# Kernel optimization log

Hardware: AMD Instinct MI355X
Metric: run time of the kernel (lower is better)

The kernel has to match this reference:

```python
import jax, jax.numpy as jnp
import numpy as np

FACTOR = 2
KERNEL_SIZE = 3
GAIN = 1


def _setup_kernel(k):
    k = np.asarray(k, dtype=np.float32)
    if k.ndim == 1:
        k = np.outer(k, k)
    k /= k.sum()
    return k


def _fir_kernel():
    # k = _setup_kernel([1,3,1]) * (gain * factor**2), shape [1,1,3,3]
    k = _setup_kernel([1, 3, 1]) * (GAIN * FACTOR ** 2)
    return jnp.asarray(k)[None, None]


def setup_inputs() -> dict:
    key = jax.random.key(0)
    k1, k2 = jax.random.split(key)
    x = jax.random.normal(k1, (16, 512, 64, 64), dtype=jnp.float32)
    w = jax.random.normal(k2, (256, 512, 3, 3), dtype=jnp.float32) * 0.05
    return {"x": x, "w": w}


def reference(x, w):
    fir = _fir_kernel()  # [1,1,3,3]
    # source uses self.k.shape[0] == 1 (unsqueezed leading dim) in the pad formula
    p = 1 - FACTOR + KERNEL_SIZE - 1          # = 1
    pad0 = (p + 1) // 2 + FACTOR - 1          # = 2
    pad1 = p // 2                              # = 0

    inC, outC, kh, kw = w.shape
    w = w.reshape(outC, inC, kh, kw)          # pure reshape (data reinterpretation), as in source

    # F.conv_transpose2d(x, w, stride=factor) == conv with lhs_dilation, flipped kernel,
    # in/out channel dims swapped, full padding (kh-1).
    w_conv = jnp.flip(w, axis=(2, 3)).transpose(1, 0, 2, 3)  # OIHW [inC, outC, kh, kw]
    x = jax.lax.conv_general_dilated(
        x, w_conv, window_strides=(1, 1),
        padding=((kh - 1, kh - 1), (kw - 1, kw - 1)),
        lhs_dilation=(FACTOR, FACTOR),
        dimension_numbers=('NCHW', 'OIHW', 'NCHW'))
    N, C, H, W = x.shape  # H = 2*H_in + 1 (odd)

    # zero-interleave block is a no-op: local factor == 1 when self.factor == 2
    x = jnp.pad(x, ((0, 0), (0, 0), (pad0, pad1), (pad0, pad1)))
    # depthwise FIR: fold channels into batch, conv with single-channel 3x3 filter
    x = x.reshape(N * C, 1, H + pad0 + pad1, W + pad0 + pad1)
    x = jax.lax.conv_general_dilated(
        x, fir, window_strides=(1, 1), padding='VALID',
        dimension_numbers=('NCHW', 'OIHW', 'NCHW'))
    x = x.reshape(N, C, H, W)

    if W % 2 != 0:  # static shape check, matches source's odd-size crop
        x = x[:, :, :W - 1, :W - 1]
    return x
```

## Files before the change

kernel.cpp:

```cpp
#include <hip/hip_runtime.h>
#include <hip/hip_bf16.h>


typedef __attribute__((ext_vector_type(8))) short short8;
typedef __attribute__((ext_vector_type(4))) float float4v;

#define XP_ELEMS ((size_t)16 * 65 * 65 * 512)
#define WP_ELEMS ((size_t)9 * 256 * 512)
#define YP_ELEMS ((size_t)4 * 16 * 256 * 4096)

__device__ __forceinline__ void gl_lds16(const __hip_bfloat16* g, __hip_bfloat16* l) {
    __builtin_amdgcn_global_load_lds(
        (const __attribute__((address_space(1))) void*)g,
        (__attribute__((address_space(3))) void*)l, 16, 0, 0);
}

__global__ __launch_bounds__(256) void zero_pad_kernel(__hip_bfloat16* __restrict__ xp) {
    int idx = blockIdx.x * 256 + (int)threadIdx.x;
    if (idx >= 16 * 65 * 512) return;
    int c = idx & 511;
    int t = (idx >> 9) % 65;
    int n = idx / (65 * 512);
    __hip_bfloat16 z = __float2bfloat16(0.f);
    xp[(((size_t)(n * 65) + 0) * 65 + t) * 512 + c] = z;
    xp[(((size_t)(n * 65) + t) * 65 + 0) * 512 + c] = z;
}

__global__ __launch_bounds__(256) void pack_w_kernel(
    const float* __restrict__ w, __hip_bfloat16* __restrict__ wp) {
    int idx = blockIdx.x * 256 + (int)threadIdx.x;
    int c  = idx & 511;
    int o  = (idx >> 9) & 255;
    int ab = idx >> 17;
    int a = ab / 3, b = ab % 3;
    wp[idx] = __float2bfloat16(w[((size_t)(c * 256 + o) * 3 + a) * 3 + b]);
}

__global__ __launch_bounds__(256) void pack_x_kernel(
    const float* __restrict__ x, __hip_bfloat16* __restrict__ xp) {
    int i = blockIdx.x;
    int n = blockIdx.y;
    int tid = (int)threadIdx.x;
    __shared__ float tile[64][65];
    for (int c0 = 0; c0 < 512; c0 += 64) {
        __syncthreads();
#pragma unroll
        for (int rr = 0; rr < 16; rr++) {
            int cl = (tid >> 6) * 16 + rr;
            int j = tid & 63;
            tile[cl][j] = x[(((size_t)(n * 512 + c0 + cl) * 64) + i) * 64 + j];
        }
        __syncthreads();
#pragma unroll
        for (int pass = 0; pass < 2; pass++) {
            int task = pass * 256 + tid;
            int j  = task >> 3;
            int cg = task & 7;
            union { short8 v; unsigned short h[8]; } u;
#pragma unroll
            for (int r = 0; r < 8; r++) {
                __hip_bfloat16 b = __float2bfloat16(tile[cg * 8 + r][j]);
                u.h[r] = *(unsigned short*)&b;
            }
            *(short8*)(xp + (((size_t)(n * 65) + i + 1) * 65 + (j + 1)) * 512 +
                       c0 + cg * 8) = u.v;
        }
    }
}

__global__ __launch_bounds__(256) void mfma_conv_kernel(
    const __hip_bfloat16* __restrict__ xp, const __hip_bfloat16* __restrict__ wp,
    __hip_bfloat16* __restrict__ yp) {
    const int p  = blockIdx.z, ph = p >> 1, pw = p & 1;
    const int o0 = blockIdx.x * 128;
    const int mt = blockIdx.y;
    const int n  = mt >> 5;
    const int i0 = (mt & 31) << 1;
    const int tid  = (int)threadIdx.x;
    const int wave = tid >> 6, lane = tid & 63;
    const int wm = wave & 1, wn = wave >> 1;
    const int lrow = lane & 15, quad = lane >> 4;
    const int m0j   = wave * 16 + (lane >> 2);
    const int klane = (lane & 3) * 8;

    __shared__ __align__(16) __hip_bfloat16 lA[128 * 32];
    __shared__ __align__(16) __hip_bfloat16 lB[128 * 32];

    float4v acc[4][4];
#pragma unroll
    for (int fm = 0; fm < 4; fm++)
#pragma unroll
        for (int fn = 0; fn < 4; fn++) acc[fm][fn] = (float4v)0.f;

    __hip_bfloat16* la0 = lA + wave * 512;
    __hip_bfloat16* la1 = lA + 2048 + wave * 512;
    __hip_bfloat16* lb0 = lB + wave * 512;
    __hip_bfloat16* lb1 = lB + 2048 + wave * 512;

    const int nrt = ph ? 1 : 2, nct = pw ? 1 : 2;
    for (int rt = 0; rt < nrt; rt++) {
        const int drp = ph ? 1 : rt;
        const int a   = ph ? 1 : (rt ? 0 : 2);
        for (int ct = 0; ct < nct; ct++) {
            const int dsp = pw ? 1 : ct;
            const int b   = pw ? 1 : (ct ? 0 : 2);
            const int ab  = a * 3 + b;
            const __hip_bfloat16* A0 =
                xp + (((size_t)(n * 65 + i0 + drp)) * 65 + m0j + dsp) * 512 + klane;
            const __hip_bfloat16* A1 = A0 + (size_t)65 * 512;
            const __hip_bfloat16* B0 =
                wp + ((size_t)(ab * 256 + o0 + m0j)) * 512 + klane;
            const __hip_bfloat16* B1 = B0 + (size_t)64 * 512;

            for (int c0 = 0; c0 < 512; c0 += 32) {
                __syncthreads();
                gl_lds16(A0 + c0, la0);
                gl_lds16(A1 + c0, la1);
                gl_lds16(B0 + c0, lb0);
                gl_lds16(B1 + c0, lb1);
                __syncthreads();
                short8 af[4], bv[4];
#pragma unroll
                for (int fm = 0; fm < 4; fm++)
                    af[fm] = *(const short8*)(lA + ((wm * 64 + fm * 16 + lrow) * 32 + quad * 8));
#pragma unroll
                for (int fn = 0; fn < 4; fn++)
                    bv[fn] = *(const short8*)(lB + ((wn * 64 + fn * 16 + lrow) * 32 + quad * 8));
#pragma unroll
                for (int fm = 0; fm < 4; fm++)
#pragma unroll
                    for (int fn = 0; fn < 4; fn++)
                        acc[fm][fn] = __builtin_amdgcn_mfma_f32_16x16x32_bf16(
                            af[fm], bv[fn], acc[fm][fn], 0, 0, 0);
            }
        }
    }

#pragma unroll
    for (int fm = 0; fm < 4; fm++) {
        int j0 = fm * 16 + quad * 4;
#pragma unroll
        for (int fn = 0; fn < 4; fn++) {
            int o = o0 + wn * 64 + fn * 16 + lrow;
            union { ushort4 v; __hip_bfloat16 h[4]; } u;
#pragma unroll
            for (int r = 0; r < 4; r++) u.h[r] = __float2bfloat16(acc[fm][fn][r]);
            *(ushort4*)(yp + (((size_t)(p * 4096 + n * 256 + o)) << 12) +
                        ((i0 + wm) << 6) + j0) = u.v;
        }
    }
}

__device__ __forceinline__ float bf_lo(unsigned u) { return __uint_as_float(u << 16); }
__device__ __forceinline__ float bf_hi(unsigned u) { return __uint_as_float(u & 0xffff0000u); }

__global__ __launch_bounds__(256) void fir_kernel(
    const __hip_bfloat16* __restrict__ yp, float* __restrict__ out) {
    const int no  = blockIdx.x;
    const int tid = (int)threadIdx.x;

    __shared__ __align__(16) unsigned short ylds[4 * 64 * 64];

    const unsigned short* ysrc = (const unsigned short*)yp;
#pragma unroll
    for (int k = 0; k < 8; k++) {
        int chunk = k * 256 + tid;
        int q   = chunk >> 9;
        int off = (chunk & 511) << 3;
        *(short8*)(ylds + q * 4096 + off) =
            *(const short8*)(ysrc + (((size_t)(q * 4096 + no)) << 12) + off);
    }
    __syncthreads();

    const unsigned* yw = (const unsigned*)ylds;

    const int qp = tid & 31;
    const int iw = tid >> 5;

    const float rw[2][2][2] = {{{0.4f, 0.4f}, {1.2f, 0.f}},
                               {{0.f, 1.2f}, {0.4f, 0.4f}}};

    for (int s = 0; s < 8; s++) {
        const int I = s * 8 + iw;

        float Y3[2][2][2][3];
#pragma unroll
        for (int q = 0; q < 4; q++) {
            int phh = q >> 1, pww = q & 1;
#pragma unroll
            for (int k = 0; k < 2; k++) {
                int ih = I - 1 + k;
                float c0 = 0.f, c1 = 0.f, c2 = 0.f;
                if (ih >= 0) {
                    const unsigned* row = yw + (q * 64 + ih) * 32;
                    unsigned wb = row[qp];
                    c1 = bf_lo(wb);
                    c2 = bf_hi(wb);
                    if (qp > 0) c0 = bf_hi(row[qp - 1]);
                }
                Y3[phh][pww][k][0] = c0;
                Y3[phh][pww][k][1] = c1;
                Y3[phh][pww][k][2] = c2;
            }
        }

        float res[2][4];
#pragma unroll
        for (int t = 0; t < 2; t++) {
            float cs[2][2][2];
#pragma unroll
            for (int phh = 0; phh < 2; phh++)
#pragma unroll
                for (int k = 0; k < 2; k++)
#pragma unroll
                    for (int ew = 0; ew < 2; ew++) {
                        float sv = 0.f;
#pragma unroll
                        for (int pww = 0; pww < 2; pww++)
#pragma unroll
                            for (int l = 0; l < 2; l++)
                                sv += rw[ew][pww][l] * Y3[phh][pww][k][t + l];
                        cs[phh][k][ew] = sv;
                    }
#pragma unroll
            for (int eh = 0; eh < 2; eh++)
#pragma unroll
                for (int ew = 0; ew < 2; ew++) {
                    float sv = 0.f;
#pragma unroll
                    for (int phh = 0; phh < 2; phh++)
#pragma unroll
                        for (int k = 0; k < 2; k++)
                            sv += rw[eh][phh][k] * cs[phh][k][ew];
                    res[eh][t * 2 + ew] = sv;
                }
        }

        size_t base = ((size_t)no << 14) + ((size_t)(2 * I) << 7) + 4 * qp;
        float4v v0 = {res[0][0], res[0][1], res[0][2], res[0][3]};
        float4v v1 = {res[1][0], res[1][1], res[1][2], res[1][3]};
        *(float4v*)(out + base)       = v0;
        *(float4v*)(out + base + 128) = v1;
    }
}

__global__ __launch_bounds__(256) void fused_direct_kernel(
    const float* __restrict__ x, const float* __restrict__ w,
    float* __restrict__ out) {
    int idx = blockIdx.x * 256 + (int)threadIdx.x;
    int w_ = idx & 127, h = (idx >> 7) & 127, no = idx >> 14;
    int o = no & 255, n = no >> 8;
    int I = h >> 1, J = w_ >> 1;
    const float fr0 = 0.4f, fr1 = 1.2f, fr2 = 0.4f;
    float gh[3][3]; int rh[3]; int nh;
    if ((h & 1) == 0) {
        nh = 3;
        rh[0] = I - 2; gh[0][0] = 0.f; gh[0][1] = 0.f; gh[0][2] = fr0;
        rh[1] = I - 1; gh[1][0] = fr0; gh[1][1] = fr1; gh[1][2] = fr2;
        rh[2] = I;     gh[2][0] = fr2; gh[2][1] = 0.f; gh[2][2] = 0.f;
    } else {
        nh = 2;
        rh[0] = I - 1; gh[0][0] = 0.f; gh[0][1] = fr0; gh[0][2] = fr1;
        rh[1] = I;     gh[1][0] = fr1; gh[1][1] = fr2; gh[1][2] = 0.f;
    }
    float gw[3][3]; int cw[3]; int nw;
    if ((w_ & 1) == 0) {
        nw = 3;
        cw[0] = J - 2; gw[0][0] = 0.f; gw[0][1] = 0.f; gw[0][2] = fr0;
        cw[1] = J - 1; gw[1][0] = fr0; gw[1][1] = fr1; gw[1][2] = fr2;
        cw[2] = J;     gw[2][0] = fr2; gw[2][1] = 0.f; gw[2][2] = 0.f;
    } else {
        nw = 2;
        cw[0] = J - 1; gw[0][0] = 0.f; gw[0][1] = fr0; gw[0][2] = fr1;
        cw[1] = J;     gw[1][0] = fr1; gw[1][1] = fr2; gw[1][2] = 0.f;
    }
    float acc = 0.f;
    for (int c = 0; c < 512; c++) {
        const float* xb = x + ((size_t)(n * 512 + c) << 12);
        const float* wb = w + (size_t)(c * 256 + o) * 9;
        float tmp[3][3];
#pragma unroll
        for (int dr = 0; dr < 3; dr++) tmp[dr][0] = tmp[dr][1] = tmp[dr][2] = 0.f;
        for (int dr = 0; dr < nh; dr++) {
            int r = rh[dr]; if (r < 0) continue;
            for (int ds = 0; ds < nw; ds++) {
                int s = cw[ds]; if (s < 0) continue;
                float xv = xb[(r << 6) + s];
                tmp[dr][0] += gw[ds][0] * xv;
                tmp[dr][1] += gw[ds][1] * xv;
                tmp[dr][2] += gw[ds][2] * xv;
            }
        }
#pragma unroll
        for (int a = 0; a < 3; a++) {
            float xg0 = 0.f, xg1 = 0.f, xg2 = 0.f;
            for (int dr = 0; dr < nh; dr++) {
                float g = gh[dr][a];
                xg0 += g * tmp[dr][0]; xg1 += g * tmp[dr][1]; xg2 += g * tmp[dr][2];
            }
            acc += xg0 * wb[a * 3] + xg1 * wb[a * 3 + 1] + xg2 * wb[a * 3 + 2];
        }
    }
    out[idx] = acc;
}

extern "C" void kernel_launch(void* const* d_in, const int* in_sizes, int n_in,
                              void* d_out, int out_size, void* d_ws, size_t ws_size,
                              hipStream_t stream)
{
    (void)in_sizes; (void)n_in; (void)out_size;
    const float* x = (const float*)d_in[0];
    const float* w = (const float*)d_in[1];
    float* out = (float*)d_out;

    const size_t need = (XP_ELEMS + WP_ELEMS + YP_ELEMS) * sizeof(__hip_bfloat16);
    if (ws_size >= need) {
        __hip_bfloat16* xp = (__hip_bfloat16*)d_ws;
        __hip_bfloat16* wp = xp + XP_ELEMS;
        __hip_bfloat16* yp = wp + WP_ELEMS;
        zero_pad_kernel<<<dim3((16 * 65 * 512 + 255) / 256), dim3(256), 0, stream>>>(xp);
        pack_w_kernel<<<dim3((int)(WP_ELEMS / 256)), dim3(256), 0, stream>>>(w, wp);
        pack_x_kernel<<<dim3(64, 16), dim3(256), 0, stream>>>(x, xp);
        mfma_conv_kernel<<<dim3(2, 512, 4), dim3(256), 0, stream>>>(xp, wp, yp);
        fir_kernel<<<dim3(4096), dim3(256), 0, stream>>>(yp, out);
    } else {
        fused_direct_kernel<<<dim3((int)(YP_ELEMS / 256)), dim3(256), 0, stream>>>(x, w, out);
    }
}
```

Baseline: 621.2 us.

## Merge prep kernels, vectorize x packing loads, remap conv grid for XCD locality

Merges the zero-pad and weight-pack kernels into one launch to save a kernel launch. pack_x now reads x with float4 loads instead of scalar loads. The conv kernel uses a flattened 1D grid with a swizzle. Consecutive block IDs, which are dealt round-robin across the 8 XCDs, then map to blocks that share the same input rows, phase and output-channel tiles, which should improve L2 reuse on each XCD. The trade-off is extra index arithmetic and dependence on how blocks are assigned to XCDs.

```diff
diff --git a/kernel.cpp b/kernel.cpp
--- a/kernel.cpp
+++ b/kernel.cpp
@@ -15,25 +15,25 @@
         (__attribute__((address_space(3))) void*)l, 16, 0, 0);
 }
 
-__global__ __launch_bounds__(256) void zero_pad_kernel(__hip_bfloat16* __restrict__ xp) {
+__global__ __launch_bounds__(256) void prep_kernel(
+    const float* __restrict__ w, __hip_bfloat16* __restrict__ wp,
+    __hip_bfloat16* __restrict__ xp) {
     int idx = blockIdx.x * 256 + (int)threadIdx.x;
-    if (idx >= 16 * 65 * 512) return;
-    int c = idx & 511;
-    int t = (idx >> 9) % 65;
-    int n = idx / (65 * 512);
-    __hip_bfloat16 z = __float2bfloat16(0.f);
-    xp[(((size_t)(n * 65) + 0) * 65 + t) * 512 + c] = z;
-    xp[(((size_t)(n * 65) + t) * 65 + 0) * 512 + c] = z;
-}
-
-__global__ __launch_bounds__(256) void pack_w_kernel(
-    const float* __restrict__ w, __hip_bfloat16* __restrict__ wp) {
-    int idx = blockIdx.x * 256 + (int)threadIdx.x;
-    int c  = idx & 511;
-    int o  = (idx >> 9) & 255;
-    int ab = idx >> 17;
-    int a = ab / 3, b = ab % 3;
-    wp[idx] = __float2bfloat16(w[((size_t)(c * 256 + o) * 3 + a) * 3 + b]);
+    {
+        int c  = idx & 511;
+        int o  = (idx >> 9) & 255;
+        int ab = idx >> 17;
+        int a = ab / 3, b = ab % 3;
+        wp[idx] = __float2bfloat16(w[((size_t)(c * 256 + o) * 3 + a) * 3 + b]);
+    }
+    if (idx < 16 * 65 * 512) {
+        int c = idx & 511;
+        int t = (idx >> 9) % 65;
+        int n = idx / (65 * 512);
+        __hip_bfloat16 z = __float2bfloat16(0.f);
+        xp[(((size_t)(n * 65) + 0) * 65 + t) * 512 + c] = z;
+        xp[(((size_t)(n * 65) + t) * 65 + 0) * 512 + c] = z;
+    }
 }
 
 __global__ __launch_bounds__(256) void pack_x_kernel(
@@ -42,13 +42,16 @@
     int n = blockIdx.y;
     int tid = (int)threadIdx.x;
     __shared__ float tile[64][65];
+    const int j4 = (tid & 15) * 4;
     for (int c0 = 0; c0 < 512; c0 += 64) {
         __syncthreads();
 #pragma unroll
-        for (int rr = 0; rr < 16; rr++) {
-            int cl = (tid >> 6) * 16 + rr;
-            int j = tid & 63;
-            tile[cl][j] = x[(((size_t)(n * 512 + c0 + cl) * 64) + i) * 64 + j];
+        for (int rr = 0; rr < 4; rr++) {
+            int cl = rr * 16 + (tid >> 4);
+            float4v v = *(const float4v*)(
+                x + (((size_t)(n * 512 + c0 + cl) * 64) + i) * 64 + j4);
+#pragma unroll
+            for (int t = 0; t < 4; t++) tile[cl][j4 + t] = v[t];
         }
         __syncthreads();
 #pragma unroll
@@ -71,9 +74,12 @@
 __global__ __launch_bounds__(256) void mfma_conv_kernel(
     const __hip_bfloat16* __restrict__ xp, const __hip_bfloat16* __restrict__ wp,
     __hip_bfloat16* __restrict__ yp) {
-    const int p  = blockIdx.z, ph = p >> 1, pw = p & 1;
-    const int o0 = blockIdx.x * 128;
-    const int mt = blockIdx.y;
+    const int flat = (int)blockIdx.x;
+    const int nf   = ((flat & 7) << 9) + (flat >> 3);
+    const int p    = nf & 3;
+    const int o0   = ((nf >> 2) & 1) * 128;
+    const int mt   = nf >> 3;
+    const int ph = p >> 1, pw = p & 1;
     const int n  = mt >> 5;
     const int i0 = (mt & 31) << 1;
     const int tid  = (int)threadIdx.x;
@@ -318,10 +324,9 @@
         __hip_bfloat16* xp = (__hip_bfloat16*)d_ws;
         __hip_bfloat16* wp = xp + XP_ELEMS;
         __hip_bfloat16* yp = wp + WP_ELEMS;
-        zero_pad_kernel<<<dim3((16 * 65 * 512 + 255) / 256), dim3(256), 0, stream>>>(xp);
-        pack_w_kernel<<<dim3((int)(WP_ELEMS / 256)), dim3(256), 0, stream>>>(w, wp);
+        prep_kernel<<<dim3((int)(WP_ELEMS / 256)), dim3(256), 0, stream>>>(w, wp, xp);
         pack_x_kernel<<<dim3(64, 16), dim3(256), 0, stream>>>(x, xp);
-        mfma_conv_kernel<<<dim3(2, 512, 4), dim3(256), 0, stream>>>(xp, wp, yp);
+        mfma_conv_kernel<<<dim3(4096), dim3(256), 0, stream>>>(xp, wp, yp);
         fir_kernel<<<dim3(4096), dim3(256), 0, stream>>>(yp, out);
     } else {
         fused_direct_kernel<<<dim3((int)(YP_ELEMS / 256)), dim3(256), 0, stream>>>(x, w, out);
```

New measurement: 679.2 us. +9.3%, slower.
